# Optimization experiments

Hardware: AMD Instinct MI355X
Metric: run time of the kernel (lower is better)

The kernel has to match this reference:

```python
import jax, jax.numpy as jnp
import numpy as np

S, D = 4096, 512      # seq_len, d_model
H, DK = 8, 64         # n_heads, dk == dv
DFF = 2048            # feed-forward hidden
EPS = 1e-5            # torch LayerNorm default eps


def _posenc(seq_len, d_model):
    # Section 3.5 encoding, matching the loop: even i -> sin(pos/10000^(i/d)),
    # odd i -> cos(pos/10000^((i-1)/d)).
    pos = jnp.arange(seq_len, dtype=jnp.float32)[:, None]
    i = jnp.arange(d_model)
    exponent = ((i - (i % 2)).astype(jnp.float32)) / d_model
    ang = pos / jnp.power(jnp.float32(10000.0), exponent)
    return jnp.where(i % 2 == 0, jnp.sin(ang), jnp.cos(ang))


def _layernorm(x, g, b):
    m = jnp.mean(x, axis=-1, keepdims=True)
    v = jnp.mean(jnp.square(x - m), axis=-1, keepdims=True)
    return (x - m) / jnp.sqrt(v + EPS) * g + b


def setup_inputs() -> dict:
    key = jax.random.key(0)
    ks = jax.random.split(key, 9)
    return {
        "E":  jax.random.normal(ks[0], (S, D), jnp.float32),
        # per-head projections stacked over head axis (original: python list of heads)
        "Wq": jax.random.normal(ks[1], (H, D, DK), jnp.float32),
        "Wk": jax.random.normal(ks[2], (H, D, DK), jnp.float32),
        "Wv": jax.random.normal(ks[3], (H, D, DK), jnp.float32),
        "WO": jax.random.normal(ks[4], (H * DK, D), jnp.float32),
        "W1": jax.random.normal(ks[5], (D, DFF), jnp.float32),
        "b1": jax.random.normal(ks[6], (DFF,), jnp.float32),
        "W2": jax.random.normal(ks[7], (DFF, D), jnp.float32),
        "b2": jax.random.normal(ks[8], (D,), jnp.float32),
        # nn.LayerNorm learned affine params (init: weight=1, bias=0)
        "g1": jnp.ones((D,), jnp.float32),
        "be1": jnp.zeros((D,), jnp.float32),
        "g2": jnp.ones((D,), jnp.float32),
        "be2": jnp.zeros((D,), jnp.float32),
    }


def reference(E, Wq, Wk, Wv, WO, W1, b1, W2, b2, g1, be1, g2, be2):
    x = E + _posenc(E.shape[0], E.shape[1])           # (S, D)
    # batched replacement for the per-head python loop
    Q = jnp.einsum('sd,hdk->hsk', x, Wq)              # (H, S, DK)
    K = jnp.einsum('sd,hdk->hsk', x, Wk)
    V = jnp.einsum('sd,hdk->hsk', x, Wv)
    att = jnp.einsum('hsk,htk->hst', Q, K) / jnp.sqrt(jnp.float32(DK))
    Z = jnp.einsum('hst,htv->hsv', jax.nn.softmax(att, axis=-1), V)  # (H,S,DK)
    Zcat = jnp.transpose(Z, (1, 0, 2)).reshape(x.shape[0], H * DK)   # concat heads
    Z1 = _layernorm(Zcat @ WO + x, g1, be1)
    Z2 = jax.nn.relu(Z1 @ W1 + b1) @ W2 + b2
    return _layernorm(Z2 + Z1, g2, be2)
```

## Files before the change

### kernel.cpp

```cpp
#include <hip/hip_runtime.h>
#include <hip/hip_bf16.h>
#include <cmath>

typedef unsigned short u16;
typedef __attribute__((ext_vector_type(8))) short short8;
typedef __attribute__((ext_vector_type(4))) float float4v;
#define LN_EPS 1e-5f

__device__ __forceinline__ float us2f(u16 u) {
    return __uint_as_float(((unsigned int)u) << 16);
}
__device__ __forceinline__ u16 f2us(float f) {
    __hip_bfloat16 h = __float2bfloat16(f);
    return *(u16*)&h;
}

__global__ __launch_bounds__(256) void sentinel_kernel(float* out, float v) {
    out[blockIdx.x * 256 + threadIdx.x] = v;
}

__global__ __launch_bounds__(256) void qkv11_kernel(const float* __restrict__ E,
                                                    const float* __restrict__ Wq,
                                                    const float* __restrict__ Wk,
                                                    const float* __restrict__ Wv,
                                                    float* __restrict__ Qcat,
                                                    u16* __restrict__ Khi,
                                                    u16* __restrict__ Klo,
                                                    u16* __restrict__ Vt,
                                                    double* __restrict__ Ftab) {
    const int h = blockIdx.y;
    const float* W0 = Wq + (long)h * 512 * 64;
    const float* W1 = Wk + (long)h * 512 * 64;
    const float* W2 = Wv + (long)h * 512 * 64;

    __shared__ u16 sAh[64][72], sAl[64][72];
    __shared__ u16 sBh[3][64][72], sBl[3][64][72];
    __shared__ double sFreqRev[512];

    const int t = threadIdx.x;
    const int w = t >> 6, l = t & 63;
    const int quad = l >> 4, l16 = l & 15;
    const int mw = w * 16;
    const int m0 = blockIdx.x * 64;

    {
        const double c = -9.210340371976184 / 512.0;
        sFreqRev[t] = exp((double)(t & ~1) * c) * 0.15915494309189535;
        sFreqRev[t + 256] =
            exp((double)((t + 256) & ~1) * c) * 0.15915494309189535;
    }
    __syncthreads();
    if (blockIdx.x == 0 && blockIdx.y == 0) {
        Ftab[t] = sFreqRev[t];
        Ftab[t + 256] = sFreqRev[t + 256];
    }

    const int ar = t >> 2, ac = (t & 3) << 4;
    const double posd = (double)(m0 + ar);
    const int brow4 = (t >> 4) << 2;
    const int bnc = (t & 15) << 2;

    float4v acc[3][4];
    #pragma unroll
    for (int ty = 0; ty < 3; ++ty)
        #pragma unroll
        for (int nt = 0; nt < 4; ++nt) acc[ty][nt] = (float4v){0.f, 0.f, 0.f, 0.f};

    for (int k0 = 0; k0 < 512; k0 += 64) {
        #pragma unroll
        for (int u = 0; u < 4; ++u) {
            float4 ev = *(const float4*)(E + (long)(m0 + ar) * 512 + k0 + ac + 4 * u);
            float xs[4] = {ev.x, ev.y, ev.z, ev.w};
            ushort4 hh, ll;
            u16* hp = (u16*)&hh; u16* lp = (u16*)&ll;
            #pragma unroll
            for (int j = 0; j < 4; ++j) {
                const int col = k0 + ac + 4 * u + j;
                double rev = posd * sFreqRev[col];
                float fr = (float)(rev - floor(rev));
                float ang = 6.28318530717958647692f * fr;
                float pe = (j & 1) ? __cosf(ang) : __sinf(ang);
                float x = xs[j] + pe;
                u16 hi = f2us(x);
                hp[j] = hi;
                lp[j] = f2us(x - us2f(hi));
            }
            *(ushort4*)&sAh[ar][ac + 4 * u] = hh;
            *(ushort4*)&sAl[ar][ac + 4 * u] = ll;
        }
        #pragma unroll
        for (int ty = 0; ty < 3; ++ty) {
            const float* W = (ty == 0 ? W0 : ty == 1 ? W1 : W2);
            float wv4[4][4];
            #pragma unroll
            for (int u = 0; u < 4; ++u)
                *(float4*)&wv4[u][0] =
                    *(const float4*)(W + (long)(k0 + brow4 + u) * 64 + bnc);
            #pragma unroll
            for (int j = 0; j < 4; ++j) {
                ushort4 hh, ll;
                #pragma unroll
                for (int u = 0; u < 4; ++u) {
                    u16 hi = f2us(wv4[u][j]);
                    ((u16*)&hh)[u] = hi;
                    ((u16*)&ll)[u] = f2us(wv4[u][j] - us2f(hi));
                }
                *(ushort4*)&sBh[ty][bnc + j][brow4] = hh;
                *(ushort4*)&sBl[ty][bnc + j][brow4] = ll;
            }
        }
        __syncthreads();
        #pragma unroll
        for (int kc = 0; kc < 2; ++kc) {
            short8 ah = *(const short8*)&sAh[mw + l16][kc * 32 + quad * 8];
            short8 al = *(const short8*)&sAl[mw + l16][kc * 32 + quad * 8];
            #pragma unroll
            for (int ty = 0; ty < 3; ++ty)
                #pragma unroll
                for (int nt = 0; nt < 4; ++nt) {
                    short8 bh = *(const short8*)&sBh[ty][nt * 16 + l16][kc * 32 + quad * 8];
                    short8 bl = *(const short8*)&sBl[ty][nt * 16 + l16][kc * 32 + quad * 8];
                    acc[ty][nt] = __builtin_amdgcn_mfma_f32_16x16x32_bf16(ah, bh, acc[ty][nt], 0, 0, 0);
                    acc[ty][nt] = __builtin_amdgcn_mfma_f32_16x16x32_bf16(ah, bl, acc[ty][nt], 0, 0, 0);
                    acc[ty][nt] = __builtin_amdgcn_mfma_f32_16x16x32_bf16(al, bh, acc[ty][nt], 0, 0, 0);
                }
        }
        __syncthreads();
    }

    #pragma unroll
    for (int nt = 0; nt < 4; ++nt)
        #pragma unroll
        for (int rr = 0; rr < 4; ++rr) {
            const int row = m0 + mw + quad * 4 + rr;
            Qcat[(long)row * 512 + h * 64 + nt * 16 + l16] = acc[0][nt][rr];
        }
    {
        const int kb = m0 >> 6;
        #pragma unroll
        for (int nt = 0; nt < 4; ++nt) {
            const int fkc = nt >> 1;
            const int fquad = ((nt & 1) << 1) + (l16 >> 3);
            const int fe = l16 & 7;
            const long fbase = ((long)(h * 64 + kb) * 8 + fkc * 4 + w) * 512 +
                               fquad * 128 + fe;
            #pragma unroll
            for (int rr = 0; rr < 4; ++rr) {
                const long off = fbase + (quad * 4 + rr) * 8;
                float v = acc[1][nt][rr];
                u16 hi = f2us(v);
                Khi[off] = hi;
                Klo[off] = f2us(v - us2f(hi));
            }
        }
    }
    {
        const int kb = m0 >> 6;
        const int fkc = w >> 1;
        const int fquad = ((w & 1) << 1) + (quad >> 1);
        const int fe0 = (quad & 1) * 4;
        #pragma unroll
        for (int nt = 0; nt < 4; ++nt) {
            const long off = ((long)(h * 64 + kb) * 8 + fkc * 4 + nt) * 512 +
                             (fquad * 16 + l16) * 8 + fe0;
            ushort4 o;
            o.x = f2us(acc[2][nt][0]); o.y = f2us(acc[2][nt][1]);
            o.z = f2us(acc[2][nt][2]); o.w = f2us(acc[2][nt][3]);
            *(ushort4*)(Vt + off) = o;
        }
    }
}

__global__ __launch_bounds__(512, 2) void flash18_kernel(const u16* __restrict__ Khi,
                                                         const u16* __restrict__ Klo,
                                                         const u16* __restrict__ Vt,
                                                         float* __restrict__ QZ) {
    const int bid = blockIdx.x;
    const int h = bid & 7;
    const int qb = bid >> 3;

    __shared__ u16 sP[8][32][72];
    __shared__ float mAcc[4][2][4][64][4];
    __shared__ float mML[4][2][2][64];

    const int t = threadIdx.x;
    const int w = t >> 6;
    const int wq = w & 3;
    const int khalf = w >> 2;
    const int l = t & 63;
    const int quad = l >> 4;
    const int l16 = l & 15;
    const int mrow0 = qb * 128 + wq * 32;

    short8 qh[2][2], ql[2][2];
    #pragma unroll
    for (int mf = 0; mf < 2; ++mf)
        #pragma unroll
        for (int kc = 0; kc < 2; ++kc) {
            const float* qp = QZ + (long)(mrow0 + mf * 16 + l16) * 512 + h * 64 +
                              kc * 32 + quad * 8;
            float4 qa = *(const float4*)qp;
            float4 qb4 = *(const float4*)(qp + 4);
            float qv[8] = {qa.x, qa.y, qa.z, qa.w, qb4.x, qb4.y, qb4.z, qb4.w};
            #pragma unroll
            for (int i = 0; i < 8; ++i) {
                float f = qv[i] * 0.125f;
                u16 hi = f2us(f);
                qh[kc][mf][i] = (short)hi;
                ql[kc][mf][i] = (short)f2us(f - us2f(hi));
            }
        }

    const u16* KH = Khi + (long)h * 262144;
    const u16* KL = Klo + (long)h * 262144;
    const u16* VT = Vt + (long)h * 262144;
    const int lo8 = l << 3;
    const int kb0 = khalf * 32;

    float m_i[2] = {-INFINITY, -INFINITY};
    float l_i[2] = {0.0f, 0.0f};
    float4v acc[2][4];
    #pragma unroll
    for (int mf = 0; mf < 2; ++mf)
        #pragma unroll
        for (int nt = 0; nt < 4; ++nt) acc[mf][nt] = (float4v){0.f, 0.f, 0.f, 0.f};

    for (int kb = kb0; kb < kb0 + 32; ++kb) {
        const long fb = (long)kb * 8;
        short8 kh_[8], kl_[8], vv_[8];
        #pragma unroll
        for (int f = 0; f < 8; ++f)
            kh_[f] = *(const short8*)(KH + (fb + f) * 512 + lo8);
        #pragma unroll
        for (int f = 0; f < 8; ++f)
            kl_[f] = *(const short8*)(KL + (fb + f) * 512 + lo8);
        #pragma unroll
        for (int f = 0; f < 8; ++f)
            vv_[f] = *(const short8*)(VT + (fb + f) * 512 + lo8);

        float4v s[2][4];
        #pragma unroll
        for (int mf = 0; mf < 2; ++mf)
            #pragma unroll
            for (int nt = 0; nt < 4; ++nt) s[mf][nt] = (float4v){0.f, 0.f, 0.f, 0.f};

        __builtin_amdgcn_s_setprio(1);
        #pragma unroll
        for (int mf = 0; mf < 2; ++mf) {
            #pragma unroll
            for (int kc = 0; kc < 2; ++kc)
                #pragma unroll
                for (int nt = 0; nt < 4; ++nt)
                    s[mf][nt] = __builtin_amdgcn_mfma_f32_16x16x32_bf16(
                        kh_[kc * 4 + nt], qh[kc][mf], s[mf][nt], 0, 0, 0);
            #pragma unroll
            for (int kc = 0; kc < 2; ++kc)
                #pragma unroll
                for (int nt = 0; nt < 4; ++nt)
                    s[mf][nt] = __builtin_amdgcn_mfma_f32_16x16x32_bf16(
                        kh_[kc * 4 + nt], ql[kc][mf], s[mf][nt], 0, 0, 0);
            #pragma unroll
            for (int kc = 0; kc < 2; ++kc)
                #pragma unroll
                for (int nt = 0; nt < 4; ++nt)
                    s[mf][nt] = __builtin_amdgcn_mfma_f32_16x16x32_bf16(
                        kl_[kc * 4 + nt], qh[kc][mf], s[mf][nt], 0, 0, 0);
        }
        __builtin_amdgcn_s_setprio(0);

        #pragma unroll
        for (int mf = 0; mf < 2; ++mf) {
            float x0 = fmaxf(fmaxf(s[mf][0][0], s[mf][0][1]),
                             fmaxf(s[mf][0][2], s[mf][0][3]));
            float x1 = fmaxf(fmaxf(s[mf][1][0], s[mf][1][1]),
                             fmaxf(s[mf][1][2], s[mf][1][3]));
            float x2 = fmaxf(fmaxf(s[mf][2][0], s[mf][2][1]),
                             fmaxf(s[mf][2][2], s[mf][2][3]));
            float x3 = fmaxf(fmaxf(s[mf][3][0], s[mf][3][1]),
                             fmaxf(s[mf][3][2], s[mf][3][3]));
            float rm = fmaxf(fmaxf(x0, x1), fmaxf(x2, x3));
            rm = fmaxf(rm, __shfl_xor(rm, 16, 64));
            rm = fmaxf(rm, __shfl_xor(rm, 32, 64));
            const float nm = fmaxf(m_i[mf], rm);
            const float al = __expf(m_i[mf] - nm);
            float p[4][4];
            #pragma unroll
            for (int nt = 0; nt < 4; ++nt)
                #pragma unroll
                for (int rr = 0; rr < 4; ++rr)
                    p[nt][rr] = __expf(s[mf][nt][rr] - nm);
            float y0 = (p[0][0] + p[0][1]) + (p[0][2] + p[0][3]);
            float y1 = (p[1][0] + p[1][1]) + (p[1][2] + p[1][3]);
            float y2 = (p[2][0] + p[2][1]) + (p[2][2] + p[2][3]);
            float y3 = (p[3][0] + p[3][1]) + (p[3][2] + p[3][3]);
            float ps = (y0 + y1) + (y2 + y3);
            ps += __shfl_xor(ps, 16, 64);
            ps += __shfl_xor(ps, 32, 64);
            l_i[mf] = l_i[mf] * al + ps;
            m_i[mf] = nm;
            #pragma unroll
            for (int nt = 0; nt < 4; ++nt) {
                acc[mf][nt][0] *= al; acc[mf][nt][1] *= al;
                acc[mf][nt][2] *= al; acc[mf][nt][3] *= al;
            }
            #pragma unroll
            for (int nt = 0; nt < 4; ++nt) {
                ushort4 pk;
                pk.x = f2us(p[nt][0]); pk.y = f2us(p[nt][1]);
                pk.z = f2us(p[nt][2]); pk.w = f2us(p[nt][3]);
                *(ushort4*)&sP[w][mf * 16 + l16][nt * 16 + quad * 4] = pk;
            }
        }

        __builtin_amdgcn_s_setprio(1);
        #pragma unroll
        for (int mf = 0; mf < 2; ++mf)
            #pragma unroll
            for (int kc = 0; kc < 2; ++kc) {
                short8 aP = *(const short8*)&sP[w][mf * 16 + l16][kc * 32 + quad * 8];
                #pragma unroll
                for (int nt = 0; nt < 4; ++nt)
                    acc[mf][nt] = __builtin_amdgcn_mfma_f32_16x16x32_bf16(
                        vv_[kc * 4 + nt], aP, acc[mf][nt], 0, 0, 0);
            }
        __builtin_amdgcn_s_setprio(0);
    }

    if (khalf == 1) {
        #pragma unroll
        for (int mf = 0; mf < 2; ++mf) {
            #pragma unroll
            for (int nt = 0; nt < 4; ++nt)
                *(float4*)&mAcc[wq][mf][nt][l][0] =
                    make_float4(acc[mf][nt][0], acc[mf][nt][1],
                                acc[mf][nt][2], acc[mf][nt][3]);
            mML[wq][mf][0][l] = m_i[mf];
            mML[wq][mf][1][l] = l_i[mf];
        }
    }
    __syncthreads();
    if (khalf == 0) {
        #pragma unroll
        for (int mf = 0; mf < 2; ++mf) {
            const float m1 = mML[wq][mf][0][l];
            const float l1 = mML[wq][mf][1][l];
            const float nm = fmaxf(m_i[mf], m1);
            const float a0 = __expf(m_i[mf] - nm);
            const float a1 = __expf(m1 - nm);
            const float inv = 1.0f / (l_i[mf] * a0 + l1 * a1);
            #pragma unroll
            for (int nt = 0; nt < 4; ++nt) {
                float4 o1 = *(float4*)&mAcc[wq][mf][nt][l][0];
                float4 o = make_float4(
                    (acc[mf][nt][0] * a0 + o1.x * a1) * inv,
                    (acc[mf][nt][1] * a0 + o1.y * a1) * inv,
                    (acc[mf][nt][2] * a0 + o1.z * a1) * inv,
                    (acc[mf][nt][3] * a0 + o1.w * a1) * inv);
                *(float4*)(QZ + (long)(mrow0 + mf * 16 + l16) * 512 + h * 64 +
                           nt * 16 + quad * 4) = o;
            }
        }
    }
}

__global__ __launch_bounds__(256) void wo2_kernel(const float* __restrict__ A,
                                                  const float* __restrict__ B,
                                                  float* __restrict__ C) {
    __shared__ u16 sAh[64][72], sAl[64][72];
    __shared__ u16 sBh[64][72], sBl[64][72];
    const int t = threadIdx.x;
    const int w = t >> 6, l = t & 63;
    const int quad = l >> 4, l16 = l & 15;
    const int mw = w * 16;
    const int m0 = blockIdx.y * 64, n0 = blockIdx.x * 64;
    const int ar = t >> 2, ac = (t & 3) << 4;

    float4v acc[4];
    #pragma unroll
    for (int nt = 0; nt < 4; ++nt) acc[nt] = (float4v){0.f, 0.f, 0.f, 0.f};

    for (int k0 = 0; k0 < 512; k0 += 64) {
        #pragma unroll
        for (int u = 0; u < 4; ++u) {
            float4 av = *(const float4*)(A + (long)(m0 + ar) * 512 + k0 + ac + 4 * u);
            float xs[4] = {av.x, av.y, av.z, av.w};
            ushort4 hh, ll;
            u16* hp = (u16*)&hh; u16* lp = (u16*)&ll;
            #pragma unroll
            for (int j = 0; j < 4; ++j) {
                u16 hi = f2us(xs[j]);
                hp[j] = hi;
                lp[j] = f2us(xs[j] - us2f(hi));
            }
            *(ushort4*)&sAh[ar][ac + 4 * u] = hh;
            *(ushort4*)&sAl[ar][ac + 4 * u] = ll;
        }
        {
            const int kr = t >> 2, nc = (t & 3) << 4;
            #pragma unroll
            for (int u = 0; u < 4; ++u) {
                float4 wv = *(const float4*)(B + (long)(k0 + kr) * 512 + n0 + nc + 4 * u);
                float ws4[4] = {wv.x, wv.y, wv.z, wv.w};
                #pragma unroll
                for (int j = 0; j < 4; ++j) {
                    const int n = nc + 4 * u + j;
                    u16 hi = f2us(ws4[j]);
                    sBh[n][kr] = hi;
                    sBl[n][kr] = f2us(ws4[j] - us2f(hi));
                }
            }
        }
        __syncthreads();
        #pragma unroll
        for (int kc = 0; kc < 2; ++kc) {
            short8 ah = *(const short8*)&sAh[mw + l16][kc * 32 + quad * 8];
            short8 al = *(const short8*)&sAl[mw + l16][kc * 32 + quad * 8];
            #pragma unroll
            for (int nt = 0; nt < 4; ++nt) {
                short8 bh = *(const short8*)&sBh[nt * 16 + l16][kc * 32 + quad * 8];
                short8 bl = *(const short8*)&sBl[nt * 16 + l16][kc * 32 + quad * 8];
                acc[nt] = __builtin_amdgcn_mfma_f32_16x16x32_bf16(ah, bh, acc[nt], 0, 0, 0);
                acc[nt] = __builtin_amdgcn_mfma_f32_16x16x32_bf16(ah, bl, acc[nt], 0, 0, 0);
                acc[nt] = __builtin_amdgcn_mfma_f32_16x16x32_bf16(al, bh, acc[nt], 0, 0, 0);
            }
        }
        __syncthreads();
    }
    #pragma unroll
    for (int nt = 0; nt < 4; ++nt)
        #pragma unroll
        for (int rr = 0; rr < 4; ++rr) {
            const int row = m0 + mw + quad * 4 + rr;
            C[(long)row * 512 + n0 + nt * 16 + l16] = acc[nt][rr];
        }
}

__global__ __launch_bounds__(256) void ln1_kernel(const float* __restrict__ tmp,
                                                  const float* __restrict__ E,
                                                  const float* __restrict__ g,
                                                  const float* __restrict__ be,
                                                  float* __restrict__ out,
                                                  u16* __restrict__ z1b,
                                                  const double* __restrict__ Ftab) {
    const int r = blockIdx.x, t = threadIdx.x;
    const long base = (long)r * 512;
    __shared__ float red[256];

    double rev0 = (double)r * Ftab[t];
    float fr0 = (float)(rev0 - floor(rev0));
    float ang0 = 6.28318530717958647692f * fr0;
    float pe0 = (t & 1) ? __cosf(ang0) : __sinf(ang0);
    double rev1 = (double)r * Ftab[t + 256];
    float fr1 = (float)(rev1 - floor(rev1));
    float ang1 = 6.28318530717958647692f * fr1;
    float pe1 = (t & 1) ? __cosf(ang1) : __sinf(ang1);

    float v0 = tmp[base + t] + E[base + t] + pe0;
    float v1 = tmp[base + t + 256] + E[base + t + 256] + pe1;

    red[t] = v0 + v1; __syncthreads();
    for (int s2 = 128; s2 > 0; s2 >>= 1) {
        if (t < s2) red[t] += red[t + s2];
        __syncthreads();
    }
    const float mean = red[0] * (1.0f / 512.0f);
    __syncthreads();
    float d0 = v0 - mean, d1 = v1 - mean;
    red[t] = d0 * d0 + d1 * d1; __syncthreads();
    for (int s2 = 128; s2 > 0; s2 >>= 1) {
        if (t < s2) red[t] += red[t + s2];
        __syncthreads();
    }
    const float rs = rsqrtf(red[0] * (1.0f / 512.0f) + LN_EPS);
    float o0 = d0 * rs * g[t] + be[t];
    float o1 = d1 * rs * g[t + 256] + be[t + 256];
    out[base + t] = o0;
    out[base + t + 256] = o1;
    z1b[base + t] = f2us(o0);
    z1b[base + t + 256] = f2us(o1);
}

__global__ __launch_bounds__(256) void wtrans_kernel(const float* __restrict__ src,
                                                     u16* __restrict__ dst,
                                                     int K, int N) {
    __shared__ float sT[64][65];
    const int t = threadIdx.x;
    const int k0 = blockIdx.x * 64, n0 = blockIdx.y * 64;
    #pragma unroll
    for (int c = 0; c < 4; ++c) {
        const int r = (t >> 4) + c * 16;
        float4 v = *(const float4*)(src + (long)(k0 + r) * N + n0 + ((t & 15) << 2));
        sT[r][((t & 15) << 2) + 0] = v.x;
        sT[r][((t & 15) << 2) + 1] = v.y;
        sT[r][((t & 15) << 2) + 2] = v.z;
        sT[r][((t & 15) << 2) + 3] = v.w;
    }
    __syncthreads();
    const int n = t >> 2, kc = (t & 3) << 4;
    #pragma unroll
    for (int u = 0; u < 4; ++u) {
        ushort4 o;
        o.x = f2us(sT[kc + 4 * u + 0][n]);
        o.y = f2us(sT[kc + 4 * u + 1][n]);
        o.z = f2us(sT[kc + 4 * u + 2][n]);
        o.w = f2us(sT[kc + 4 * u + 3][n]);
        *(ushort4*)(dst + (long)(n0 + n) * K + k0 + kc + 4 * u) = o;
    }
}

__global__ __launch_bounds__(256) void ffn1_kernel(const u16* __restrict__ A,
                                                   const u16* __restrict__ Bt,
                                                   const float* __restrict__ b1,
                                                   u16* __restrict__ C,
                                                   int m_base) {
    __shared__ u16 sA[64][72], sB[64][72];
    const int t = threadIdx.x;
    const int w = t >> 6, l = t & 63, quad = l >> 4, l16 = l & 15;
    const int mw = w * 16;
    const int m0 = m_base + blockIdx.y * 64, n0 = blockIdx.x * 64;
    const int r = t >> 2, cc = (t & 3) << 4;

    float4v acc[4];
    #pragma unroll
    for (int nt = 0; nt < 4; ++nt) acc[nt] = (float4v){0.f, 0.f, 0.f, 0.f};

    for (int kt = 0; kt < 512; kt += 64) {
        const long aoff = (long)(m0 + r) * 512 + kt + cc;
        *(uint4*)&sA[r][cc]     = *(const uint4*)(A + aoff);
        *(uint4*)&sA[r][cc + 8] = *(const uint4*)(A + aoff + 8);
        const long boff = (long)(n0 + r) * 512 + kt + cc;
        *(uint4*)&sB[r][cc]     = *(const uint4*)(Bt + boff);
        *(uint4*)&sB[r][cc + 8] = *(const uint4*)(Bt + boff + 8);
        __syncthreads();
        #pragma unroll
        for (int kc = 0; kc < 2; ++kc) {
            short8 a = *(const short8*)&sA[mw + l16][kc * 32 + quad * 8];
            #pragma unroll
            for (int nt = 0; nt < 4; ++nt) {
                short8 b = *(const short8*)&sB[nt * 16 + l16][kc * 32 + quad * 8];
                acc[nt] = __builtin_amdgcn_mfma_f32_16x16x32_bf16(a, b, acc[nt], 0, 0, 0);
            }
        }
        __syncthreads();
    }
    #pragma unroll
    for (int rr = 0; rr < 4; ++rr) {
        const int row = blockIdx.y * 64 + mw + quad * 4 + rr;
        #pragma unroll
        for (int nt = 0; nt < 4; ++nt) {
            const int col = n0 + nt * 16 + l16;
            float v = acc[nt][rr] + b1[col];
            C[(long)row * 2048 + col] = f2us(fmaxf(v, 0.0f));
        }
    }
}

__global__ __launch_bounds__(256) void ffn2_kernel(const u16* __restrict__ A,
                                                   const u16* __restrict__ Bt,
                                                   const float* __restrict__ b2,
                                                   float* __restrict__ U) {
    __shared__ u16 sA[32][72], sB[64][72];
    const int t = threadIdx.x;
    const int w = t >> 6, l = t & 63, quad = l >> 4, l16 = l & 15;
    const int mf = (w & 1) << 4;
    const int nh = (w >> 1) << 5;
    const int m0 = blockIdx.y * 32, n0 = blockIdx.x * 64;
    const int ra = t >> 3, ca = (t & 7) << 3;
    const int rb = t >> 2, cb = (t & 3) << 4;

    float4v acc[2];
    acc[0] = (float4v){0.f, 0.f, 0.f, 0.f};
    acc[1] = (float4v){0.f, 0.f, 0.f, 0.f};

    for (int kt = 0; kt < 2048; kt += 64) {
        *(uint4*)&sA[ra][ca] =
            *(const uint4*)(A + (long)(m0 + ra) * 2048 + kt + ca);
        const long boff = (long)(n0 + rb) * 2048 + kt + cb;
        *(uint4*)&sB[rb][cb]     = *(const uint4*)(Bt + boff);
        *(uint4*)&sB[rb][cb + 8] = *(const uint4*)(Bt + boff + 8);
        __syncthreads();
        #pragma unroll
        for (int kc = 0; kc < 2; ++kc) {
            short8 a = *(const short8*)&sA[mf + l16][kc * 32 + quad * 8];
            #pragma unroll
            for (int nt = 0; nt < 2; ++nt) {
                short8 b = *(const short8*)&sB[nh + nt * 16 + l16][kc * 32 + quad * 8];
                acc[nt] = __builtin_amdgcn_mfma_f32_16x16x32_bf16(a, b, acc[nt], 0, 0, 0);
            }
        }
        __syncthreads();
    }
    #pragma unroll
    for (int rr = 0; rr < 4; ++rr) {
        const int row = m0 + mf + quad * 4 + rr;
        #pragma unroll
        for (int nt = 0; nt < 2; ++nt) {
            const int col = n0 + nh + nt * 16 + l16;
            U[(long)row * 512 + col] = acc[nt][rr] + b2[col];
        }
    }
}

__global__ __launch_bounds__(256) void ln2_kernel(const float* __restrict__ U,
                                                  const float* __restrict__ Z1,
                                                  const float* __restrict__ g,
                                                  const float* __restrict__ be,
                                                  float* __restrict__ out) {
    const int r = blockIdx.x, t = threadIdx.x;
    const long base = (long)r * 512;
    __shared__ float red[256];

    float v0 = U[base + t] + Z1[base + t];
    float v1 = U[base + t + 256] + Z1[base + t + 256];

    red[t] = v0 + v1; __syncthreads();
    for (int s2 = 128; s2 > 0; s2 >>= 1) {
        if (t < s2) red[t] += red[t + s2];
        __syncthreads();
    }
    const float mean = red[0] * (1.0f / 512.0f);
    __syncthreads();
    float d0 = v0 - mean, d1 = v1 - mean;
    red[t] = d0 * d0 + d1 * d1; __syncthreads();
    for (int s2 = 128; s2 > 0; s2 >>= 1) {
        if (t < s2) red[t] += red[t + s2];
        __syncthreads();
    }
    const float rs = rsqrtf(red[0] * (1.0f / 512.0f) + LN_EPS);
    out[base + t] = d0 * rs * g[t] + be[t];
    out[base + t + 256] = d1 * rs * g[t + 256] + be[t + 256];
}

extern "C" void kernel_launch(void* const* d_in, const int* in_sizes, int n_in,
                              void* d_out, int out_size, void* d_ws, size_t ws_size,
                              hipStream_t stream) {
    float* outf = (float*)d_out;

    static const int exp_sizes[13] = {2097152, 262144, 262144, 262144, 262144,
                                      1048576, 2048, 1048576, 512, 512, 512,
                                      512, 512};
    bool ok = (n_in == 13) && (out_size == 2097152) &&
              (ws_size >= (14ull << 20));
    if (ok) for (int i = 0; i < 13; ++i) if (in_sizes[i] != exp_sizes[i]) ok = false;
    if (!ok) { sentinel_kernel<<<16, 256, 0, stream>>>(outf, 1000.0f); return; }

    const float* E   = (const float*)d_in[0];
    const float* Wq  = (const float*)d_in[1];
    const float* Wk  = (const float*)d_in[2];
    const float* Wv  = (const float*)d_in[3];
    const float* WO  = (const float*)d_in[4];
    const float* W1  = (const float*)d_in[5];
    const float* b1  = (const float*)d_in[6];
    const float* W2  = (const float*)d_in[7];
    const float* b2  = (const float*)d_in[8];
    const float* g1  = (const float*)d_in[9];
    const float* be1 = (const float*)d_in[10];
    const float* g2  = (const float*)d_in[11];
    const float* be2 = (const float*)d_in[12];

    char* base = (char*)d_ws;
    u16*   Khi = (u16*)base;
    u16*   Klo = (u16*)(base + (4l << 20));
    u16*   Vt  = (u16*)(base + (8l << 20));
    double* Ftab = (double*)(base + (12l << 20));
    float* tmp = (float*)base;
    u16*   Z1b = (u16*)(base + (8l << 20));
    u16*   W1t = (u16*)base;
    u16*   W2t = (u16*)(base + (2l << 20));
    u16*   Hff = (u16*)(base + (4l << 20));
    float* U   = (float*)(base + (12l << 20));

    qkv11_kernel<<<dim3(64, 8), 256, 0, stream>>>(E, Wq, Wk, Wv, outf,
                                                  Khi, Klo, Vt, Ftab);
    flash18_kernel<<<dim3(256), 512, 0, stream>>>(Khi, Klo, Vt, outf);
    wo2_kernel<<<dim3(8, 64), 256, 0, stream>>>(outf, WO, tmp);
    ln1_kernel<<<4096, 256, 0, stream>>>(tmp, E, g1, be1, outf, Z1b, Ftab);
    wtrans_kernel<<<dim3(8, 32), 256, 0, stream>>>(W1, W1t, 512, 2048);
    wtrans_kernel<<<dim3(32, 8), 256, 0, stream>>>(W2, W2t, 2048, 512);

    for (int c = 0; c < 4; ++c) {
        ffn1_kernel<<<dim3(32, 16), 256, 0, stream>>>(Z1b, W1t, b1, Hff,
                                                      c * 1024);
        ffn2_kernel<<<dim3(8, 32), 256, 0, stream>>>(Hff, W2t, b2, U);
        ln2_kernel<<<1024, 256, 0, stream>>>(U, outf + (long)c * 1024 * 512,
                                             g2, be2,
                                             outf + (long)c * 1024 * 512);
    }
}
```

Baseline: 369.9 us.

## Split flash attention keys four ways with smaller query tiles per block

Each flash-attention block now covers 64 query rows with four warp groups each processing a quarter of the keys, instead of 128 rows split across two key halves, so the grid doubles to 512 blocks. Partial softmax states from three sections are merged through a shared buffer aliased over the P scratch space. This aims to fill more compute units and shorten per-block latency, at the cost of less K/V reuse per loaded tile and an extra barrier plus merge work.

```diff
diff --git a/kernel.cpp b/kernel.cpp
--- a/kernel.cpp
+++ b/kernel.cpp
@@ -171,7 +171,7 @@
     }
 }
 
-__global__ __launch_bounds__(512, 2) void flash18_kernel(const u16* __restrict__ Khi,
+__global__ __launch_bounds__(512, 2) void flash19_kernel(const u16* __restrict__ Khi,
                                                          const u16* __restrict__ Klo,
                                                          const u16* __restrict__ Vt,
                                                          float* __restrict__ QZ) {
@@ -179,18 +179,19 @@
     const int h = bid & 7;
     const int qb = bid >> 3;
 
-    __shared__ u16 sP[8][32][72];
-    __shared__ float mAcc[4][2][4][64][4];
-    __shared__ float mML[4][2][2][64];
+    __shared__ __align__(16) char smem[55296];
+    u16 (*sP)[32][72] = reinterpret_cast<u16(*)[32][72]>(smem);
+    float* mAccF = (float*)smem;
+    float* mMLF = (float*)(smem + 49152);
 
     const int t = threadIdx.x;
     const int w = t >> 6;
-    const int wq = w & 3;
-    const int khalf = w >> 2;
+    const int wq = w & 1;
+    const int ksec = w >> 1;
     const int l = t & 63;
     const int quad = l >> 4;
     const int l16 = l & 15;
-    const int mrow0 = qb * 128 + wq * 32;
+    const int mrow0 = qb * 64 + wq * 32;
 
     short8 qh[2][2], ql[2][2];
     #pragma unroll
@@ -215,7 +216,7 @@
     const u16* KL = Klo + (long)h * 262144;
     const u16* VT = Vt + (long)h * 262144;
     const int lo8 = l << 3;
-    const int kb0 = khalf * 32;
+    const int kb0 = ksec * 16;
 
     float m_i[2] = {-INFINITY, -INFINITY};
     float l_i[2] = {0.0f, 0.0f};
@@ -225,7 +226,7 @@
         #pragma unroll
         for (int nt = 0; nt < 4; ++nt) acc[mf][nt] = (float4v){0.f, 0.f, 0.f, 0.f};
 
-    for (int kb = kb0; kb < kb0 + 32; ++kb) {
+    for (int kb = kb0; kb < kb0 + 16; ++kb) {
         const long fb = (long)kb * 8;
         short8 kh_[8], kl_[8], vv_[8];
         #pragma unroll
@@ -326,36 +327,56 @@
         __builtin_amdgcn_s_setprio(0);
     }
 
-    if (khalf == 1) {
+    __syncthreads();
+
+    if (ksec >= 1) {
+        const int pub = ksec - 1;
         #pragma unroll
         for (int mf = 0; mf < 2; ++mf) {
+            const int bse = ((pub * 2 + wq) * 2 + mf);
             #pragma unroll
             for (int nt = 0; nt < 4; ++nt)
-                *(float4*)&mAcc[wq][mf][nt][l][0] =
+                *(float4*)&mAccF[((bse * 4 + nt) * 64 + l) * 4] =
                     make_float4(acc[mf][nt][0], acc[mf][nt][1],
                                 acc[mf][nt][2], acc[mf][nt][3]);
-            mML[wq][mf][0][l] = m_i[mf];
-            mML[wq][mf][1][l] = l_i[mf];
+            mMLF[(bse * 2 + 0) * 64 + l] = m_i[mf];
+            mMLF[(bse * 2 + 1) * 64 + l] = l_i[mf];
         }
     }
     __syncthreads();
-    if (khalf == 0) {
+    if (ksec == 0) {
         #pragma unroll
         for (int mf = 0; mf < 2; ++mf) {
-            const float m1 = mML[wq][mf][0][l];
-            const float l1 = mML[wq][mf][1][l];
-            const float nm = fmaxf(m_i[mf], m1);
+            float nm = m_i[mf];
+            #pragma unroll
+            for (int pub = 0; pub < 3; ++pub) {
+                const int bse = ((pub * 2 + wq) * 2 + mf);
+                nm = fmaxf(nm, mMLF[(bse * 2 + 0) * 64 + l]);
+            }
             const float a0 = __expf(m_i[mf] - nm);
-            const float a1 = __expf(m1 - nm);
-            const float inv = 1.0f / (l_i[mf] * a0 + l1 * a1);
+            float lsum = l_i[mf] * a0;
+            float ax[3];
+            #pragma unroll
+            for (int pub = 0; pub < 3; ++pub) {
+                const int bse = ((pub * 2 + wq) * 2 + mf);
+                ax[pub] = __expf(mMLF[(bse * 2 + 0) * 64 + l] - nm);
+                lsum += mMLF[(bse * 2 + 1) * 64 + l] * ax[pub];
+            }
+            const float inv = 1.0f / lsum;
             #pragma unroll
             for (int nt = 0; nt < 4; ++nt) {
-                float4 o1 = *(float4*)&mAcc[wq][mf][nt][l][0];
-                float4 o = make_float4(
-                    (acc[mf][nt][0] * a0 + o1.x * a1) * inv,
-                    (acc[mf][nt][1] * a0 + o1.y * a1) * inv,
-                    (acc[mf][nt][2] * a0 + o1.z * a1) * inv,
-                    (acc[mf][nt][3] * a0 + o1.w * a1) * inv);
+                float ox = acc[mf][nt][0] * a0;
+                float oy = acc[mf][nt][1] * a0;
+                float oz = acc[mf][nt][2] * a0;
+                float ow = acc[mf][nt][3] * a0;
+                #pragma unroll
+                for (int pub = 0; pub < 3; ++pub) {
+                    const int bse = ((pub * 2 + wq) * 2 + mf);
+                    float4 o1 = *(float4*)&mAccF[((bse * 4 + nt) * 64 + l) * 4];
+                    ox += o1.x * ax[pub]; oy += o1.y * ax[pub];
+                    oz += o1.z * ax[pub]; ow += o1.w * ax[pub];
+                }
+                float4 o = make_float4(ox * inv, oy * inv, oz * inv, ow * inv);
                 *(float4*)(QZ + (long)(mrow0 + mf * 16 + l16) * 512 + h * 64 +
                            nt * 16 + quad * 4) = o;
             }
@@ -672,7 +693,7 @@
 
     qkv11_kernel<<<dim3(64, 8), 256, 0, stream>>>(E, Wq, Wk, Wv, outf,
                                                   Khi, Klo, Vt, Ftab);
-    flash18_kernel<<<dim3(256), 512, 0, stream>>>(Khi, Klo, Vt, outf);
+    flash19_kernel<<<dim3(512), 512, 0, stream>>>(Khi, Klo, Vt, outf);
     wo2_kernel<<<dim3(8, 64), 256, 0, stream>>>(outf, WO, tmp);
     ln1_kernel<<<4096, 256, 0, stream>>>(tmp, E, g1, be1, outf, Z1b, Ftab);
     wtrans_kernel<<<dim3(8, 32), 256, 0, stream>>>(W1, W1t, 512, 2048);
```

After: 373.7 us. Within noise of the previous version (+1.0%).
